# Optimization experiments

Measured on AMD Instinct MI355X. Metric: run time of the kernel, lower is better.

The kernel has to match this reference:

```python
import jax, jax.numpy as jnp
import numpy as np

N, E, DIN, H, HEADS = 50000, 800000, 128, 64, 4


def setup_inputs() -> dict:
    key = jax.random.key(0)
    ks = jax.random.split(key, 12)

    def p(k, shape, fan_in):
        return jax.random.normal(k, shape, dtype=jnp.float32) / np.float32(np.sqrt(fan_in))

    return dict(
        x=jax.random.normal(ks[0], (N, DIN), dtype=jnp.float32),
        edge_index=jax.random.randint(ks[1], (2, E), 0, N, dtype=jnp.int32),
        # GCNConv(input_dim, hidden)
        W_gcn=p(ks[2], (DIN, H), DIN), b_gcn=jnp.zeros((H,), jnp.float32),
        # GATConv(hidden, hidden, heads=4, concat=True)
        W_gat=p(ks[3], (H, HEADS * H), H),
        att_src=p(ks[4], (HEADS, H), H), att_dst=p(ks[5], (HEADS, H), H),
        b_gat=jnp.zeros((HEADS * H,), jnp.float32),
        # SAGEConv(4*hidden, hidden): lin_l (neighbors, with bias), lin_r (root, no bias)
        W_sage_l=p(ks[6], (HEADS * H, H), HEADS * H), b_sage=jnp.zeros((H,), jnp.float32),
        W_sage_r=p(ks[7], (HEADS * H, H), HEADS * H),
        # edge-pair MLP: Linear(2*hidden, hidden) -> ReLU -> Linear(hidden, 1)
        W1=p(ks[8], (2 * H, H), 2 * H), b1=jnp.zeros((H,), jnp.float32),
        W2=p(ks[9], (H, 1), H), b2=jnp.zeros((1,), jnp.float32),
    )


def reference(x, edge_index, W_gcn, b_gcn, W_gat, att_src, att_dst, b_gat,
              W_sage_l, b_sage, W_sage_r, W1, b1, W2, b2):
    n = x.shape[0]
    src, dst = edge_index[0], edge_index[1]
    loop = jnp.arange(n, dtype=edge_index.dtype)
    # edges with self-loops appended (GCN and GAT add self-loops by default)
    s2 = jnp.concatenate([src, loop])
    d2 = jnp.concatenate([dst, loop])

    h = x @ W_gcn                                            # [N, H]
    deg = jax.ops.segment_sum(jnp.ones_like(d2, jnp.float32), d2, num_segments=n)
    dinv = jnp.where(deg > 0, jax.lax.rsqrt(jnp.maximum(deg, 1e-12)), 0.0)
    norm = dinv[s2] * dinv[d2]                               # [E+N]
    h = jax.ops.segment_sum(h[s2] * norm[:, None], d2, num_segments=n) + b_gcn
    h = jax.nn.relu(h)                                       # dropout: identity in eval

    # ---- GATConv (heads=4, concat=True, negative_slope=0.2) ----
    g = (h @ W_gat).reshape(n, HEADS, H)                     # [N, heads, C]
    a_s = jnp.sum(g * att_src, axis=-1)                      # [N, heads]
    a_d = jnp.sum(g * att_dst, axis=-1)
    e = jax.nn.leaky_relu(a_s[s2] + a_d[d2], 0.2)            # [E+N, heads]
    m = jax.ops.segment_max(e, d2, num_segments=n)           # per-target max (stable softmax)
    e = jnp.exp(e - m[d2])
    z = jax.ops.segment_sum(e, d2, num_segments=n)
    alpha = e / (z[d2] + 1e-16)                              # edge softmax over incoming edges
    g = jax.ops.segment_sum(g[s2] * alpha[:, :, None], d2, num_segments=n)
    g = jax.nn.relu(g.reshape(n, HEADS * H) + b_gat)

    # ---- SAGEConv (mean aggregation, root weight, no self-loops) ----
    nsum = jax.ops.segment_sum(g[src], dst, num_segments=n)
    cnt = jax.ops.segment_sum(jnp.ones_like(dst, jnp.float32), dst, num_segments=n)
    mean = nsum / jnp.maximum(cnt, 1.0)[:, None]
    s = jax.nn.relu(mean @ W_sage_l + b_sage + g @ W_sage_r)  # [N, H]

    # ---- edge-pair MLP + sigmoid ----
    ef = jnp.concatenate([s[src], s[dst]], axis=1)            # [E, 2H]
    pred = jax.nn.relu(ef @ W1 + b1) @ W2 + b2                # [E, 1]
    return jax.nn.sigmoid(pred[:, 0])
```

## Files before the change

### kernel.cpp

```cpp
#include <hip/hip_runtime.h>
#include <math.h>

typedef float v2f __attribute__((ext_vector_type(2)));
static __device__ __forceinline__ float4 f4s(float v){ return make_float4(v,v,v,v); }
static __device__ __forceinline__ float4 f4add(float4 a, float4 b){ return make_float4(a.x+b.x,a.y+b.y,a.z+b.z,a.w+b.w); }
static __device__ __forceinline__ float4 f4max(float4 a, float4 b){ return make_float4(fmaxf(a.x,b.x),fmaxf(a.y,b.y),fmaxf(a.z,b.z),fmaxf(a.w,b.w)); }
static __device__ __forceinline__ float4 f4scale(float4 a, float s){ return make_float4(a.x*s,a.y*s,a.z*s,a.w*s); }
static __device__ __forceinline__ float4 f4fma(float4 acc, float s, float4 b){
  acc.x += s*b.x; acc.y += s*b.y; acc.z += s*b.z; acc.w += s*b.w; return acc;
}
static __device__ __forceinline__ float4 f4relu(float4 a){ return f4max(a, f4s(0.f)); }
static __device__ __forceinline__ float4 f4leaky(float4 a){
  return make_float4(a.x>0.f?a.x:0.2f*a.x, a.y>0.f?a.y:0.2f*a.y, a.z>0.f?a.z:0.2f*a.z, a.w>0.f?a.w:0.2f*a.w);
}
static __device__ __forceinline__ float4 f4expf(float4 a){ return make_float4(__expf(a.x),__expf(a.y),__expf(a.z),__expf(a.w)); }
static __device__ __forceinline__ unsigned short f2bf(float f){
  unsigned int u = __float_as_uint(f);
  unsigned int r = (u + 0x7fffu + ((u >> 16) & 1u)) >> 16;
  return (unsigned short)r;
}
static __device__ __forceinline__ ushort4 f2bf4(float4 f){
  ushort4 r; r.x=f2bf(f.x); r.y=f2bf(f.y); r.z=f2bf(f.z); r.w=f2bf(f.w); return r;
}
static __device__ __forceinline__ float4 bfu2f4(uint2 u){
  return make_float4(__uint_as_float(u.x << 16), __uint_as_float(u.x & 0xffff0000u),
                     __uint_as_float(u.y << 16), __uint_as_float(u.y & 0xffff0000u));
}
static __device__ __forceinline__ float4 bfu2f4_lo(uint4 u){ return bfu2f4(make_uint2(u.x, u.y)); }
static __device__ __forceinline__ float4 bfu2f4_hi(uint4 u){ return bfu2f4(make_uint2(u.z, u.w)); }

typedef __attribute__((ext_vector_type(8))) unsigned short u16x8;
static __device__ __forceinline__ u16x8 f2bf8(float4 a, float4 b){
  u16x8 r;
  r[0]=f2bf(a.x); r[1]=f2bf(a.y); r[2]=f2bf(a.z); r[3]=f2bf(a.w);
  r[4]=f2bf(b.x); r[5]=f2bf(b.y); r[6]=f2bf(b.z); r[7]=f2bf(b.w);
  return r;
}
static __device__ __forceinline__ void red2(float4& a, float4& b){
  a.x += __shfl_xor(a.x, 8); a.y += __shfl_xor(a.y, 8);
  a.z += __shfl_xor(a.z, 8); a.w += __shfl_xor(a.w, 8);
  b.x += __shfl_xor(b.x, 8); b.y += __shfl_xor(b.y, 8);
  b.z += __shfl_xor(b.z, 8); b.w += __shfl_xor(b.w, 8);
}
static __device__ __forceinline__ unsigned char f2fp8(float v){
  return (unsigned char)(__builtin_amdgcn_cvt_pk_fp8_f32(v, v, 0, false) & 0xff);
}
static __device__ __forceinline__ unsigned int f4_fp8x4(float4 v){
  unsigned int r = __builtin_amdgcn_cvt_pk_fp8_f32(v.x, v.y, 0, false);
  r = __builtin_amdgcn_cvt_pk_fp8_f32(v.z, v.w, r, true);
  return r;
}
static __device__ __forceinline__ float4 fp8x4_f4(unsigned int q){
  v2f lo = __builtin_amdgcn_cvt_pk_f32_fp8(q, false);
  v2f hi = __builtin_amdgcn_cvt_pk_f32_fp8(q, true);
  return make_float4(lo[0], lo[1], hi[0], hi[1]);
}
static __device__ __forceinline__ float dot8(float4 a, float4 b, const float* v){
  return a.x*v[0]+a.y*v[1]+a.z*v[2]+a.w*v[3]+b.x*v[4]+b.y*v[5]+b.z*v[6]+b.w*v[7];
}

typedef __attribute__((ext_vector_type(8))) short bf16x8;
typedef __attribute__((ext_vector_type(4))) float f32x4;

__global__ __launch_bounds__(256) void k_rank(const int* __restrict__ dst, int* __restrict__ cnt,
                                              int* __restrict__ rank, int E){
  int t = blockIdx.x*256 + threadIdx.x;
  if (t < E) rank[t] = atomicAdd(&cnt[dst[t]], 1);
}
__global__ __launch_bounds__(256) void k_scan1v(const int* __restrict__ cnt, int* __restrict__ excl,
                                                int* __restrict__ bsum, int n, int nb,
                                                const float* __restrict__ Wg, const float* __restrict__ as,
                                                const float* __restrict__ ad, float* __restrict__ Vs,
                                                float* __restrict__ Vd){
  if ((int)blockIdx.x == nb){
    int t = threadIdx.x;
    int h = t >> 6, k = t & 63;
    float s = 0.f, d = 0.f;
    const float* wr = Wg + (size_t)k*256 + h*64;
    const float* ar = as + h*64;
    const float* dr = ad + h*64;
    for (int c = 0; c < 64; ++c){ float w = wr[c]; s += w*ar[c]; d += w*dr[c]; }
    Vs[t] = s; Vd[t] = d;
    return;
  }
  __shared__ int sc[256];
  int t = threadIdx.x; int i = blockIdx.x*256 + t;
  int v = (i<n)?cnt[i]:0;
  sc[t]=v; __syncthreads();
  for (int o=1;o<256;o<<=1){ int a=(t>=o)?sc[t-o]:0; __syncthreads(); sc[t]+=a; __syncthreads(); }
  if (i<n) excl[i] = sc[t]-v;
  if (t==255) bsum[blockIdx.x] = sc[t];
}
__global__ __launch_bounds__(256) void k_scan3b(const int* __restrict__ cnt, const int* __restrict__ excl,
                                                const int* __restrict__ bsum, int* __restrict__ offs,
                                                float* __restrict__ dinv, int n, int E, int nb){
  __shared__ int sb[256];
  int t = threadIdx.x;
  int v = (t<nb)?bsum[t]:0;
  sb[t]=v; __syncthreads();
  for (int o=1;o<256;o<<=1){ int a=(t>=o)?sb[t-o]:0; __syncthreads(); sb[t]+=a; __syncthreads(); }
  int bex = sb[blockIdx.x] - bsum[blockIdx.x];
  int i = blockIdx.x*256 + t;
  if (i < n){
    offs[i] = excl[i] + bex;
    dinv[i] = rsqrtf((float)cnt[i] + 1.0f);
    if (i == 0) offs[n] = E;
  }
}

__global__ __launch_bounds__(256) void k_fillg(const int* __restrict__ src, const int* __restrict__ dstv,
                                               const int* __restrict__ offs, const int* __restrict__ rank,
                                               int* __restrict__ csr, int E, int fb,
                                               const float* __restrict__ x, const float* __restrict__ Wg,
                                               unsigned char* __restrict__ a8, int n,
                                               const float* __restrict__ dinv){
  if ((int)blockIdx.x < fb){
    int t = blockIdx.x*256 + threadIdx.x;
    if (t < E) csr[offs[dstv[t]] + rank[t]] = src[t];
    return;
  }
  __shared__ unsigned short wb[1024*8];
  int tid = threadIdx.x;
  for (int s = tid; s < 1024; s += 256){
    int l = s & 63, f = s >> 6;
    int cc = f & 3, kb = f >> 2;
    int c  = cc*16 + (l & 15);
    int kr = kb*32 + ((l >> 4) << 3);
    const float* wp = Wg + (size_t)kr*64 + c;
    unsigned short* dp = &wb[s*8];
    #pragma unroll
    for (int j = 0; j < 8; ++j) dp[j] = f2bf(wp[(size_t)j*64]);
  }
  __syncthreads();
  int wv = tid >> 6, l = tid & 63;
  int lrow = l & 15;
  int lk = (l >> 4) << 3;
  int g = blockIdx.x - fb;
  int r0 = (g << 6) + (wv << 4);
  int m = r0 + lrow;
  bf16x8 afr[4];
  #pragma unroll
  for (int kb = 0; kb < 4; ++kb){
    bf16x8 a = {0,0,0,0,0,0,0,0};
    if (m < n){
      const float* p = x + (size_t)m*128 + kb*32 + lk;
      float4 f0 = *(const float4*)p;
      float4 f1 = *(const float4*)(p + 4);
      a[0]=(short)f2bf(f0.x); a[1]=(short)f2bf(f0.y); a[2]=(short)f2bf(f0.z); a[3]=(short)f2bf(f0.w);
      a[4]=(short)f2bf(f1.x); a[5]=(short)f2bf(f1.y); a[6]=(short)f2bf(f1.z); a[7]=(short)f2bf(f1.w);
    }
    afr[kb] = a;
  }
  int rbase = r0 + ((l >> 4) << 2);
  float sc[4];
  #pragma unroll
  for (int r = 0; r < 4; ++r) sc[r] = (rbase + r < n) ? dinv[rbase + r] : 0.f;
  #pragma unroll
  for (int cc = 0; cc < 4; ++cc){
    f32x4 acc = {0.f, 0.f, 0.f, 0.f};
    #pragma unroll
    for (int kb = 0; kb < 4; ++kb){
      bf16x8 b = *(const bf16x8*)&wb[((kb*4 + cc)*64 + l)*8];
      acc = __builtin_amdgcn_mfma_f32_16x16x32_bf16(afr[kb], b, acc, 0, 0, 0);
    }
    int c = cc*16 + lrow;
    #pragma unroll
    for (int r = 0; r < 4; ++r){
      int rr = rbase + r;
      if (rr < n) a8[(size_t)rr*64 + c] = f2fp8(acc[r] * sc[r]);
    }
  }
}

__global__ __launch_bounds__(256) void k_gatsage(const unsigned short* __restrict__ Y,
                                                 const float* __restrict__ Wg,
                                                 const float* __restrict__ bg,
                                                 const float* __restrict__ Wl,
                                                 const float* __restrict__ Wr,
                                                 unsigned short* __restrict__ R,
                                                 unsigned char* __restrict__ P8, int n){
  constexpr int LDG = 264;
  extern __shared__ unsigned short lds[];
  unsigned short* wb1 = lds;
  unsigned short* wb2 = wb1 + 2048*8;
  unsigned short* gb  = wb2 + 4096*8;
  int tid = threadIdx.x;
  for (int s = tid; s < 2048; s += 256){
    int l = s & 63, f = s >> 6;
    int cc = f & 15, kb = f >> 4;
    int c  = cc*16 + (l & 15);
    int kr = kb*32 + ((l >> 4) << 3);
    const float* wp = Wg + (size_t)kr*256 + c;
    unsigned short* dp = &wb1[s*8];
    #pragma unroll
    for (int j = 0; j < 8; ++j) dp[j] = f2bf(wp[(size_t)j*256]);
  }
  for (int s = tid; s < 4096; s += 256){
    int l = s & 63, f = s >> 6;
    int cc = f & 7, kb = f >> 3;
    int c  = cc*16 + (l & 15);
    int kr = kb*32 + ((l >> 4) << 3);
    const float* wp = (c >= 64) ? (Wr + (size_t)kr*64 + (c - 64)) : (Wl + (size_t)kr*64 + c);
    unsigned short* dp = &wb2[s*8];
    #pragma unroll
    for (int j = 0; j < 8; ++j) dp[j] = f2bf(wp[(size_t)j*64]);
  }
  __syncthreads();
  int wv = tid >> 6, l = tid & 63;
  int lrow = l & 15;
  int lk = (l >> 4) << 3;
  int rbase4 = (l >> 4) << 2;
  int ngrp = (n + 63) >> 6;
  for (int g = blockIdx.x; g < ngrp; g += gridDim.x){
    int r0 = (g << 6) + (wv << 4);
    int m = r0 + lrow;
    bf16x8 afr[4][2];
    #pragma unroll
    for (int h = 0; h < 4; ++h){
      #pragma unroll
      for (int kb = 0; kb < 2; ++kb){
        bf16x8 a = {0,0,0,0,0,0,0,0};
        if (m < n) a = *(const bf16x8*)(Y + (size_t)m*256 + h*64 + kb*32 + lk);
        afr[h][kb] = a;
      }
    }
    #pragma unroll
    for (int cc = 0; cc < 16; ++cc){
      f32x4 acc = {0.f, 0.f, 0.f, 0.f};
      int hh = cc >> 2;
      #pragma unroll
      for (int kb = 0; kb < 2; ++kb){
        bf16x8 b = *(const bf16x8*)&wb1[((kb*16 + cc)*64 + l)*8];
        acc = __builtin_amdgcn_mfma_f32_16x16x32_bf16(afr[hh][kb], b, acc, 0, 0, 0);
      }
      int c = cc*16 + lrow;
      float bv = bg[c];
      #pragma unroll
      for (int r = 0; r < 4; ++r){
        int lr = (wv << 4) + rbase4 + r;
        gb[lr*LDG + c] = f2bf(fmaxf(acc[r] + bv, 0.f));
      }
    }
    bf16x8 afb[8];
    #pragma unroll
    for (int kb = 0; kb < 8; ++kb)
      afb[kb] = *(const bf16x8*)&gb[((wv << 4) + lrow)*LDG + kb*32 + lk];
    #pragma unroll
    for (int cc = 0; cc < 8; ++cc){
      f32x4 acc = {0.f, 0.f, 0.f, 0.f};
      #pragma unroll
      for (int kb = 0; kb < 8; ++kb){
        bf16x8 b = *(const bf16x8*)&wb2[((kb*8 + cc)*64 + l)*8];
        acc = __builtin_amdgcn_mfma_f32_16x16x32_bf16(afb[kb], b, acc, 0, 0, 0);
      }
      int c = cc*16 + lrow;
      #pragma unroll
      for (int r = 0; r < 4; ++r){
        int rr = r0 + rbase4 + r;
        if (rr < n){
          float v = acc[r];
          if (c < 64) P8[(size_t)rr*64 + c] = f2fp8(v);
          else        R[(size_t)rr*64 + (c - 64)] = f2bf(v);
        }
      }
    }
  }
}

__global__ __launch_bounds__(256) void k_gcn(const unsigned char* __restrict__ a8, const float* __restrict__ dinv,
                                             const float* __restrict__ b, const int* __restrict__ offs,
                                             const int* __restrict__ csr, const float* __restrict__ Vs,
                                             const float* __restrict__ Vd, unsigned char* __restrict__ h8,
                                             float* __restrict__ D, int n){
  __shared__ float svs[256], svd[256];
  svs[threadIdx.x] = Vs[threadIdx.x];
  svd[threadIdx.x] = Vd[threadIdx.x];
  __syncthreads();
  int l = threadIdx.x & 63;
  int node = (((blockIdx.x*256 + threadIdx.x) >> 6) << 2) + (l >> 4);
  int l15 = l & 15;
  int grp = l15 >> 3, sub = l15 & 7;
  bool ok = node < n;
  int beg = 0, end = 0;
  float di = 0.f;
  if (ok){ beg = offs[node]; end = offs[node+1]; di = dinv[node]; }
  float4 aL0 = f4s(0.f), aH0 = f4s(0.f), aL1 = f4s(0.f), aH1 = f4s(0.f);
  int i = beg + grp;
  for (; i + 2 < end; i += 4){
    int s0 = csr[i], s1 = csr[i+2];
    uint2 u0 = *(const uint2*)(a8 + (size_t)s0*64 + (sub<<3));
    uint2 u1 = *(const uint2*)(a8 + (size_t)s1*64 + (sub<<3));
    aL0 = f4add(aL0, fp8x4_f4(u0.x)); aH0 = f4add(aH0, fp8x4_f4(u0.y));
    aL1 = f4add(aL1, fp8x4_f4(u1.x)); aH1 = f4add(aH1, fp8x4_f4(u1.y));
  }
  if (i < end){
    int s0 = csr[i];
    uint2 u0 = *(const uint2*)(a8 + (size_t)s0*64 + (sub<<3));
    aL0 = f4add(aL0, fp8x4_f4(u0.x)); aH0 = f4add(aH0, fp8x4_f4(u0.y));
  }
  float4 aL = f4add(aL0, aL1), aH = f4add(aH0, aH1);
  red2(aL, aH);
  if (ok){
    uint2 us = *(const uint2*)(a8 + (size_t)node*64 + (sub<<3));
    aL = f4add(aL, fp8x4_f4(us.x)); aH = f4add(aH, fp8x4_f4(us.y));
    float4 b0 = *(const float4*)(b + (sub<<3));
    float4 b1 = *(const float4*)(b + (sub<<3) + 4);
    float4 r0 = f4relu(f4fma(b0, di, aL));
    float4 r1 = f4relu(f4fma(b1, di, aH));
    if (grp == 0){
      uint2 q; q.x = f4_fp8x4(r0); q.y = f4_fp8x4(r1);
      *(uint2*)(h8 + (size_t)node*64 + (sub<<3)) = q;
    }
    const float* vs0 = svs + (grp*128) + (sub<<3);
    const float* vd0 = svd + (grp*128) + (sub<<3);
    float s0 = dot8(r0, r1, vs0);
    float s1 = dot8(r0, r1, vs0 + 64);
    float d0 = dot8(r0, r1, vd0);
    float d1 = dot8(r0, r1, vd0 + 64);
    #pragma unroll
    for (int o = 1; o < 8; o <<= 1){
      s0 += __shfl_xor(s0, o); s1 += __shfl_xor(s1, o);
      d0 += __shfl_xor(d0, o); d1 += __shfl_xor(d1, o);
    }
    if (sub == 0){
      *(float2*)(D + (size_t)node*8 + grp*2)     = make_float2(s0, s1);
      *(float2*)(D + (size_t)node*8 + 4 + grp*2) = make_float2(d0, d1);
    }
  }
}

#define GAT_CAP 128
__global__ __launch_bounds__(256) void k_gat2(const float* __restrict__ D, const unsigned char* __restrict__ H8,
                                              const int* __restrict__ offs, const int* __restrict__ csr,
                                              unsigned short* __restrict__ Y, int n){
  __shared__ float wl[8][GAT_CAP*4];
  __shared__ int   sl[8][GAT_CAP];
  int hw = threadIdx.x >> 5;
  int node = (blockIdx.x*256 + threadIdx.x) >> 5;
  int l5 = threadIdx.x & 31;
  if (node >= n) return;
  int beg = offs[node], end = offs[node+1];
  int deg = end - beg;
  float4 ed  = *(const float4*)(D + (size_t)node*8 + 4);
  float4 es0 = *(const float4*)(D + (size_t)node*8);
  float4 wself = f4expf(f4leaky(f4add(es0, ed)));
  float4 z4 = f4s(0.f);
  for (int i = beg + l5; i < end; i += 32){
    int s = csr[i];
    float4 w = f4expf(f4leaky(f4add(*(const float4*)(D + (size_t)s*8), ed)));
    int li = i - beg;
    if (li < GAT_CAP){ *(float4*)&wl[hw][li<<2] = w; sl[hw][li] = s << 6; }
    z4 = f4add(z4, w);
  }
  for (int m = 1; m < 32; m <<= 1){
    z4.x += __shfl_xor(z4.x, m); z4.y += __shfl_xor(z4.y, m);
    z4.z += __shfl_xor(z4.z, m); z4.w += __shfl_xor(z4.w, m);
  }
  z4 = f4add(z4, wself);
  int grp = l5 >> 4;
  int sub = l5 & 15;
  int c0b = sub << 2;
  float4 a0 = f4s(0.f), a1 = f4s(0.f), a2 = f4s(0.f), a3 = f4s(0.f);
  int nl = deg < GAT_CAP ? deg : GAT_CAP;
  int i = grp;
  for (; i + 2 < nl; i += 4){
    int o0 = sl[hw][i], o1 = sl[hw][i+2];
    float4 w0 = *(const float4*)&wl[hw][i<<2];
    float4 w1 = *(const float4*)&wl[hw][(i+2)<<2];
    unsigned int q0 = *(const unsigned int*)(H8 + o0 + c0b);
    unsigned int q1 = *(const unsigned int*)(H8 + o1 + c0b);
    float4 f0 = fp8x4_f4(q0);
    float4 f1 = fp8x4_f4(q1);
    a0 = f4fma(a0, w0.x, f0); a1 = f4fma(a1, w0.y, f0);
    a2 = f4fma(a2, w0.z, f0); a3 = f4fma(a3, w0.w, f0);
    a0 = f4fma(a0, w1.x, f1); a1 = f4fma(a1, w1.y, f1);
    a2 = f4fma(a2, w1.z, f1); a3 = f4fma(a3, w1.w, f1);
  }
  if (i < nl){
    float4 w0 = *(const float4*)&wl[hw][i<<2];
    float4 f0 = fp8x4_f4(*(const unsigned int*)(H8 + sl[hw][i] + c0b));
    a0 = f4fma(a0, w0.x, f0); a1 = f4fma(a1, w0.y, f0);
    a2 = f4fma(a2, w0.z, f0); a3 = f4fma(a3, w0.w, f0);
  }
  for (int j = nl + grp; j < deg; j += 2){
    int s = csr[beg+j];
    float4 e = f4leaky(f4add(*(const float4*)(D + (size_t)s*8), ed));
    float4 w = f4expf(e);
    float4 f0 = fp8x4_f4(*(const unsigned int*)(H8 + ((size_t)s << 6) + c0b));
    a0 = f4fma(a0, w.x, f0); a1 = f4fma(a1, w.y, f0);
    a2 = f4fma(a2, w.z, f0); a3 = f4fma(a3, w.w, f0);
  }
  a0.x += __shfl_xor(a0.x, 16); a0.y += __shfl_xor(a0.y, 16); a0.z += __shfl_xor(a0.z, 16); a0.w += __shfl_xor(a0.w, 16);
  a1.x += __shfl_xor(a1.x, 16); a1.y += __shfl_xor(a1.y, 16); a1.z += __shfl_xor(a1.z, 16); a1.w += __shfl_xor(a1.w, 16);
  a2.x += __shfl_xor(a2.x, 16); a2.y += __shfl_xor(a2.y, 16); a2.z += __shfl_xor(a2.z, 16); a2.w += __shfl_xor(a2.w, 16);
  a3.x += __shfl_xor(a3.x, 16); a3.y += __shfl_xor(a3.y, 16); a3.z += __shfl_xor(a3.z, 16); a3.w += __shfl_xor(a3.w, 16);
  if (grp == 0){
    float4 fs = fp8x4_f4(*(const unsigned int*)(H8 + ((size_t)node << 6) + c0b));
    a0 = f4fma(a0, wself.x, fs);
    a1 = f4fma(a1, wself.y, fs);
    a2 = f4fma(a2, wself.z, fs);
    a3 = f4fma(a3, wself.w, fs);
    a0 = f4scale(a0, 1.f/(z4.x + 1e-16f));
    a1 = f4scale(a1, 1.f/(z4.y + 1e-16f));
    a2 = f4scale(a2, 1.f/(z4.z + 1e-16f));
    a3 = f4scale(a3, 1.f/(z4.w + 1e-16f));
    unsigned short* yp = Y + (size_t)node*256 + (sub << 2);
    *(ushort4*)(yp)       = f2bf4(a0);
    *(ushort4*)(yp + 64)  = f2bf4(a1);
    *(ushort4*)(yp + 128) = f2bf4(a2);
    *(ushort4*)(yp + 192) = f2bf4(a3);
  }
}

__global__ __launch_bounds__(256) void k_sage(const unsigned char* __restrict__ P8, const unsigned short* __restrict__ R,
                                              const float* __restrict__ b, const int* __restrict__ offs,
                                              const int* __restrict__ csr, const float* __restrict__ W1a,
                                              const float* __restrict__ W1b, unsigned char* __restrict__ T2, int n){
  __shared__ unsigned short wfr[1024*8];
  __shared__ unsigned short stile[16][72];
  int tid = threadIdx.x;
  for (int s = tid; s < 1024; s += 256){
    int l = s & 63, f = s >> 6;
    int cc = f & 7, kb = f >> 3;
    int c  = cc*16 + (l & 15);
    int kr = kb*32 + ((l >> 4) << 3);
    const float* wp = (c >= 64) ? (W1b + (size_t)kr*64 + (c - 64)) : (W1a + (size_t)kr*64 + c);
    unsigned short* dp = &wfr[s*8];
    #pragma unroll
    for (int j = 0; j < 8; ++j) dp[j] = f2bf(wp[(size_t)j*64]);
  }
  int wv = tid >> 6, l = tid & 63;
  int base = blockIdx.x*16;
  int lrow16 = (wv << 2) + (l >> 4);
  int node = base + lrow16;
  int l15 = l & 15;
  int grp = l15 >> 3, sub = l15 & 7;
  bool ok = node < n;
  int beg = 0, end = 0;
  if (ok){ beg = offs[node]; end = offs[node+1]; }
  float4 aL0 = f4s(0.f), aH0 = f4s(0.f), aL1 = f4s(0.f), aH1 = f4s(0.f);
  int i = beg + grp;
  for (; i + 2 < end; i += 4){
    int s0 = csr[i], s1 = csr[i+2];
    uint2 u0 = *(const uint2*)(P8 + (size_t)s0*64 + (sub<<3));
    uint2 u1 = *(const uint2*)(P8 + (size_t)s1*64 + (sub<<3));
    aL0 = f4add(aL0, fp8x4_f4(u0.x)); aH0 = f4add(aH0, fp8x4_f4(u0.y));
    aL1 = f4add(aL1, fp8x4_f4(u1.x)); aH1 = f4add(aH1, fp8x4_f4(u1.y));
  }
  if (i < end){
    int s0 = csr[i];
    uint2 u0 = *(const uint2*)(P8 + (size_t)s0*64 + (sub<<3));
    aL0 = f4add(aL0, fp8x4_f4(u0.x)); aH0 = f4add(aH0, fp8x4_f4(u0.y));
  }
  float4 aL = f4add(aL0, aL1), aH = f4add(aH0, aH1);
  red2(aL, aH);
  float4 r0 = f4s(0.f), r1 = f4s(0.f);
  if (ok){
    float minv = 1.f / fmaxf((float)(end - beg), 1.f);
    uint4 ur = *(const uint4*)(R + (size_t)node*64 + (sub<<3));
    float4 b0 = *(const float4*)(b + (sub<<3));
    float4 b1 = *(const float4*)(b + (sub<<3) + 4);
    r0 = f4relu(f4add(f4fma(b0, minv, aL), bfu2f4_lo(ur)));
    r1 = f4relu(f4add(f4fma(b1, minv, aH), bfu2f4_hi(ur)));
  }
  if (grp == 0) *(u16x8*)&stile[lrow16][sub << 3] = f2bf8(r0, r1);
  __syncthreads();
  int lrow = l & 15, lk = (l >> 4) << 3;
  bf16x8 af0 = *(const bf16x8*)&stile[lrow][lk];
  bf16x8 af1 = *(const bf16x8*)&stile[lrow][32 + lk];
  int rbase = (l >> 4) << 2;
  #pragma unroll
  for (int q = 0; q < 2; ++q){
    int cc = wv*2 + q;
    f32x4 acc = {0.f, 0.f, 0.f, 0.f};
    acc = __builtin_amdgcn_mfma_f32_16x16x32_bf16(af0, *(const bf16x8*)&wfr[(cc*64 + l)*8], acc, 0, 0, 0);
    acc = __builtin_amdgcn_mfma_f32_16x16x32_bf16(af1, *(const bf16x8*)&wfr[((8 + cc)*64 + l)*8], acc, 0, 0, 0);
    int c = cc*16 + lrow;
    #pragma unroll
    for (int r = 0; r < 4; ++r){
      int nd = base + rbase + r;
      if (nd < n) T2[(size_t)nd*128 + c] = f2fp8(acc[r]);
    }
  }
}

__global__ __launch_bounds__(256) void k_mlp(const unsigned char* __restrict__ T2,
                                             const float* __restrict__ b1, const float* __restrict__ W2,
                                             const float* __restrict__ b2, const int* __restrict__ src,
                                             const int* __restrict__ dst, float* __restrict__ out, int E){
  int t = threadIdx.x;
  int e = blockIdx.x*32 + (t >> 3);
  if (e >= E) return;
  int sub = t & 7;
  int s = src[e], d = dst[e];
  uint2 uu = *(const uint2*)(T2 + (size_t)s*128 + (sub<<3));
  uint2 vv = *(const uint2*)(T2 + (size_t)d*128 + 64 + (sub<<3));
  float4 u0 = fp8x4_f4(uu.x), u1 = fp8x4_f4(uu.y);
  float4 v0 = fp8x4_f4(vv.x), v1 = fp8x4_f4(vv.y);
  float4 bb0 = *(const float4*)(b1 + (sub<<3));
  float4 bb1 = *(const float4*)(b1 + (sub<<3) + 4);
  float4 w0 = *(const float4*)(W2 + (sub<<3));
  float4 w1 = *(const float4*)(W2 + (sub<<3) + 4);
  float4 ta = f4relu(f4add(f4add(u0, v0), bb0));
  float4 tb = f4relu(f4add(f4add(u1, v1), bb1));
  float p = ta.x*w0.x + ta.y*w0.y + ta.z*w0.z + ta.w*w0.w
          + tb.x*w1.x + tb.y*w1.y + tb.z*w1.z + tb.w*w1.w;
  p += __shfl_xor(p, 1);
  p += __shfl_xor(p, 2);
  p += __shfl_xor(p, 4);
  if (sub == 0) out[e] = 1.f / (1.f + __expf(-(p + b2[0])));
}

extern "C" void kernel_launch(void* const* d_in, const int* in_sizes, int n_in,
                              void* d_out, int out_size, void* d_ws, size_t ws_size,
                              hipStream_t stream){
  const float* x     = (const float*)d_in[0];
  const int*   eidx  = (const int*)  d_in[1];
  const float* W_gcn = (const float*)d_in[2];
  const float* b_gcn = (const float*)d_in[3];
  const float* W_gat = (const float*)d_in[4];
  const float* att_s = (const float*)d_in[5];
  const float* att_d = (const float*)d_in[6];
  const float* b_gat = (const float*)d_in[7];
  const float* W_sl  = (const float*)d_in[8];
  const float* b_sg  = (const float*)d_in[9];
  const float* W_sr  = (const float*)d_in[10];
  const float* W1    = (const float*)d_in[11];
  const float* b1    = (const float*)d_in[12];
  const float* W2    = (const float*)d_in[13];
  const float* b2    = (const float*)d_in[14];
  float* out = (float*)d_out;

  const int N = in_sizes[0] / 128;
  const int E = in_sizes[1] / 2;
  const int* src = eidx;
  const int* dst = eidx + E;

  float* ws   = (float*)d_ws;
  float* dinv = ws;
  float* D    = dinv + (size_t)N;
  float* Vs   = D + (size_t)N*8;
  float* Vd   = Vs + 256;
  unsigned short* Y  = (unsigned short*)(Vd + 256);
  unsigned short* R  = Y + (size_t)N*256;
  unsigned char*  A8 = (unsigned char*)(R + (size_t)N*64);
  unsigned char*  H8 = A8 + (size_t)N*64;
  unsigned char*  P8 = H8 + (size_t)N*64;
  unsigned char*  T2 = P8 + (size_t)N*64;
  int* cnt  = (int*)(T2 + (size_t)N*128);
  int* excl = cnt + N;
  int* bsum = excl + N;
  int* offs = bsum + 256;
  int* rank = offs + N + 1;
  int* csr  = rank + E;

  const int nb = (N + 255) / 256;
  const int fb = (E + 255) / 256;
  const int gtiles = (N + 63) / 64;
  const int nwb = (N + 15) / 16;
  const int GSH = (2048*8 + 4096*8 + 64*264) * 2;

  static bool s_attr = false;
  if (!s_attr){
    hipFuncSetAttribute((const void*)k_gatsage, hipFuncAttributeMaxDynamicSharedMemorySize, GSH);
    s_attr = true;
  }

  hipMemsetAsync(cnt, 0, (size_t)N*sizeof(int), stream);
  k_rank  <<<fb, 256, 0, stream>>>(dst, cnt, rank, E);
  k_scan1v<<<nb + 1, 256, 0, stream>>>(cnt, excl, bsum, N, nb, W_gat, att_s, att_d, Vs, Vd);
  k_scan3b<<<nb, 256, 0, stream>>>(cnt, excl, bsum, offs, dinv, N, E, nb);
  k_fillg <<<fb + gtiles, 256, 0, stream>>>(src, dst, offs, rank, csr, E, fb,
                                            x, W_gcn, A8, N, dinv);

  k_gcn <<<nwb, 256, 0, stream>>>(A8, dinv, b_gcn, offs, csr, Vs, Vd, H8, D, N);

  k_gat2<<<(N+7)/8, 256, 0, stream>>>(D, H8, offs, csr, Y, N);

  k_gatsage<<<256, 256, GSH, stream>>>(Y, W_gat, b_gat, W_sl, W_sr, R, P8, N);

  k_sage<<<nwb, 256, 0, stream>>>(P8, R, b_sg, offs, csr, W1, W1 + 64*64, T2, N);

  k_mlp <<<(E+31)/32, 256, 0, stream>>>(T2, b1, W2, b2, src, dst, out, E);
}
```

Before: 285.6 us.

## Pre-pack GAT/SAGE weights to bf16 once and read them from global memory

The bf16 conversion and fragment packing of the GAT and SAGE weight matrices moves into extra blocks of the rank kernel, writing the packed layout to workspace once. k_gatsage no longer stages ~96KB of weights in LDS per block. It reads B fragments straight from global/L2 and keeps only a small LDS tile, so one 64-row tile per block over 782 blocks with higher occupancy. The cost is repeated global reads of weight fragments instead of LDS reads.

```diff
diff --git a/kernel.cpp b/kernel.cpp
--- a/kernel.cpp
+++ b/kernel.cpp
@@ -62,11 +62,37 @@
 typedef __attribute__((ext_vector_type(8))) short bf16x8;
 typedef __attribute__((ext_vector_type(4))) float f32x4;
 
-__global__ __launch_bounds__(256) void k_rank(const int* __restrict__ dst, int* __restrict__ cnt,
-                                              int* __restrict__ rank, int E){
-  int t = blockIdx.x*256 + threadIdx.x;
-  if (t < E) rank[t] = atomicAdd(&cnt[dst[t]], 1);
-}
+__global__ __launch_bounds__(256) void k_rankw(const int* __restrict__ dst, int* __restrict__ cnt,
+                                               int* __restrict__ rank, int E, int fb,
+                                               const float* __restrict__ Wg, const float* __restrict__ Wl,
+                                               const float* __restrict__ Wr, unsigned short* __restrict__ WT){
+  if ((int)blockIdx.x < fb){
+    int t = blockIdx.x*256 + threadIdx.x;
+    if (t < E) rank[t] = atomicAdd(&cnt[dst[t]], 1);
+    return;
+  }
+  int s = (blockIdx.x - fb)*256 + threadIdx.x;
+  int l = s & 63, f = s >> 6;
+  const float* wp; int ld;
+  if (s < 2048){
+    int cc = f & 15, kb = f >> 4;
+    int c  = cc*16 + (l & 15);
+    int kr = kb*32 + ((l >> 4) << 3);
+    wp = Wg + (size_t)kr*256 + c; ld = 256;
+  } else {
+    int f2 = f - 32;
+    int cc = f2 & 7, kb = f2 >> 3;
+    int c  = cc*16 + (l & 15);
+    int kr = kb*32 + ((l >> 4) << 3);
+    wp = (c >= 64) ? (Wr + (size_t)kr*64 + (c - 64)) : (Wl + (size_t)kr*64 + c);
+    ld = 64;
+  }
+  u16x8 o;
+  #pragma unroll
+  for (int j = 0; j < 8; ++j) o[j] = f2bf(wp[(size_t)j*ld]);
+  *(u16x8*)(WT + (size_t)s*8) = o;
+}
+
 __global__ __launch_bounds__(256) void k_scan1v(const int* __restrict__ cnt, int* __restrict__ excl,
                                                 int* __restrict__ bsum, int n, int nb,
                                                 const float* __restrict__ Wg, const float* __restrict__ as,
@@ -172,96 +198,69 @@
   }
 }
 
-__global__ __launch_bounds__(256) void k_gatsage(const unsigned short* __restrict__ Y,
-                                                 const float* __restrict__ Wg,
-                                                 const float* __restrict__ bg,
-                                                 const float* __restrict__ Wl,
-                                                 const float* __restrict__ Wr,
-                                                 unsigned short* __restrict__ R,
-                                                 unsigned char* __restrict__ P8, int n){
+__global__ __launch_bounds__(256, 4) void k_gatsage(const unsigned short* __restrict__ Y,
+                                                    const unsigned short* __restrict__ WT,
+                                                    const float* __restrict__ bg,
+                                                    unsigned short* __restrict__ R,
+                                                    unsigned char* __restrict__ P8, int n){
   constexpr int LDG = 264;
-  extern __shared__ unsigned short lds[];
-  unsigned short* wb1 = lds;
-  unsigned short* wb2 = wb1 + 2048*8;
-  unsigned short* gb  = wb2 + 4096*8;
+  __shared__ unsigned short gb[64*LDG];
+  const unsigned short* WT1 = WT;
+  const unsigned short* WT2 = WT + 2048*8;
   int tid = threadIdx.x;
-  for (int s = tid; s < 2048; s += 256){
-    int l = s & 63, f = s >> 6;
-    int cc = f & 15, kb = f >> 4;
-    int c  = cc*16 + (l & 15);
-    int kr = kb*32 + ((l >> 4) << 3);
-    const float* wp = Wg + (size_t)kr*256 + c;
-    unsigned short* dp = &wb1[s*8];
-    #pragma unroll
-    for (int j = 0; j < 8; ++j) dp[j] = f2bf(wp[(size_t)j*256]);
-  }
-  for (int s = tid; s < 4096; s += 256){
-    int l = s & 63, f = s >> 6;
-    int cc = f & 7, kb = f >> 3;
-    int c  = cc*16 + (l & 15);
-    int kr = kb*32 + ((l >> 4) << 3);
-    const float* wp = (c >= 64) ? (Wr + (size_t)kr*64 + (c - 64)) : (Wl + (size_t)kr*64 + c);
-    unsigned short* dp = &wb2[s*8];
-    #pragma unroll
-    for (int j = 0; j < 8; ++j) dp[j] = f2bf(wp[(size_t)j*64]);
-  }
-  __syncthreads();
   int wv = tid >> 6, l = tid & 63;
   int lrow = l & 15;
   int lk = (l >> 4) << 3;
   int rbase4 = (l >> 4) << 2;
-  int ngrp = (n + 63) >> 6;
-  for (int g = blockIdx.x; g < ngrp; g += gridDim.x){
-    int r0 = (g << 6) + (wv << 4);
-    int m = r0 + lrow;
-    bf16x8 afr[4][2];
-    #pragma unroll
-    for (int h = 0; h < 4; ++h){
-      #pragma unroll
-      for (int kb = 0; kb < 2; ++kb){
-        bf16x8 a = {0,0,0,0,0,0,0,0};
-        if (m < n) a = *(const bf16x8*)(Y + (size_t)m*256 + h*64 + kb*32 + lk);
-        afr[h][kb] = a;
-      }
-    }
-    #pragma unroll
-    for (int cc = 0; cc < 16; ++cc){
-      f32x4 acc = {0.f, 0.f, 0.f, 0.f};
-      int hh = cc >> 2;
-      #pragma unroll
-      for (int kb = 0; kb < 2; ++kb){
-        bf16x8 b = *(const bf16x8*)&wb1[((kb*16 + cc)*64 + l)*8];
-        acc = __builtin_amdgcn_mfma_f32_16x16x32_bf16(afr[hh][kb], b, acc, 0, 0, 0);
-      }
-      int c = cc*16 + lrow;
-      float bv = bg[c];
-      #pragma unroll
-      for (int r = 0; r < 4; ++r){
-        int lr = (wv << 4) + rbase4 + r;
-        gb[lr*LDG + c] = f2bf(fmaxf(acc[r] + bv, 0.f));
-      }
-    }
-    bf16x8 afb[8];
-    #pragma unroll
-    for (int kb = 0; kb < 8; ++kb)
-      afb[kb] = *(const bf16x8*)&gb[((wv << 4) + lrow)*LDG + kb*32 + lk];
-    #pragma unroll
-    for (int cc = 0; cc < 8; ++cc){
-      f32x4 acc = {0.f, 0.f, 0.f, 0.f};
-      #pragma unroll
-      for (int kb = 0; kb < 8; ++kb){
-        bf16x8 b = *(const bf16x8*)&wb2[((kb*8 + cc)*64 + l)*8];
-        acc = __builtin_amdgcn_mfma_f32_16x16x32_bf16(afb[kb], b, acc, 0, 0, 0);
-      }
-      int c = cc*16 + lrow;
-      #pragma unroll
-      for (int r = 0; r < 4; ++r){
-        int rr = r0 + rbase4 + r;
-        if (rr < n){
-          float v = acc[r];
-          if (c < 64) P8[(size_t)rr*64 + c] = f2fp8(v);
-          else        R[(size_t)rr*64 + (c - 64)] = f2bf(v);
-        }
+  int r0 = ((int)blockIdx.x << 6) + (wv << 4);
+  int m = r0 + lrow;
+  bf16x8 afr[4][2];
+  #pragma unroll
+  for (int h = 0; h < 4; ++h){
+    #pragma unroll
+    for (int kb = 0; kb < 2; ++kb){
+      bf16x8 a = {0,0,0,0,0,0,0,0};
+      if (m < n) a = *(const bf16x8*)(Y + (size_t)m*256 + h*64 + kb*32 + lk);
+      afr[h][kb] = a;
+    }
+  }
+  #pragma unroll
+  for (int cc = 0; cc < 16; ++cc){
+    f32x4 acc = {0.f, 0.f, 0.f, 0.f};
+    int hh = cc >> 2;
+    #pragma unroll
+    for (int kb = 0; kb < 2; ++kb){
+      bf16x8 b = *(const bf16x8*)&WT1[((size_t)((kb*16 + cc)*64 + l))*8];
+      acc = __builtin_amdgcn_mfma_f32_16x16x32_bf16(afr[hh][kb], b, acc, 0, 0, 0);
+    }
+    int c = cc*16 + lrow;
+    float bv = bg[c];
+    #pragma unroll
+    for (int r = 0; r < 4; ++r){
+      int lr = (wv << 4) + rbase4 + r;
+      gb[lr*LDG + c] = f2bf(fmaxf(acc[r] + bv, 0.f));
+    }
+  }
+  bf16x8 afb[8];
+  #pragma unroll
+  for (int kb = 0; kb < 8; ++kb)
+    afb[kb] = *(const bf16x8*)&gb[((wv << 4) + lrow)*LDG + kb*32 + lk];
+  #pragma unroll
+  for (int cc = 0; cc < 8; ++cc){
+    f32x4 acc = {0.f, 0.f, 0.f, 0.f};
+    #pragma unroll
+    for (int kb = 0; kb < 8; ++kb){
+      bf16x8 b = *(const bf16x8*)&WT2[((size_t)((kb*8 + cc)*64 + l))*8];
+      acc = __builtin_amdgcn_mfma_f32_16x16x32_bf16(afb[kb], b, acc, 0, 0, 0);
+    }
+    int c = cc*16 + lrow;
+    #pragma unroll
+    for (int r = 0; r < 4; ++r){
+      int rr = r0 + rbase4 + r;
+      if (rr < n){
+        float v = acc[r];
+        if (c < 64) P8[(size_t)rr*64 + c] = f2fp8(v);
+        else        R[(size_t)rr*64 + (c - 64)] = f2bf(v);
       }
     }
   }
@@ -541,7 +540,8 @@
   float* D    = dinv + (size_t)N;
   float* Vs   = D + (size_t)N*8;
   float* Vd   = Vs + 256;
-  unsigned short* Y  = (unsigned short*)(Vd + 256);
+  unsigned short* WT = (unsigned short*)(Vd + 256);
+  unsigned short* Y  = WT + (size_t)6144*8;
   unsigned short* R  = Y + (size_t)N*256;
   unsigned char*  A8 = (unsigned char*)(R + (size_t)N*64);
   unsigned char*  H8 = A8 + (size_t)N*64;
@@ -558,16 +558,9 @@
   const int fb = (E + 255) / 256;
   const int gtiles = (N + 63) / 64;
   const int nwb = (N + 15) / 16;
-  const int GSH = (2048*8 + 4096*8 + 64*264) * 2;
-
-  static bool s_attr = false;
-  if (!s_attr){
-    hipFuncSetAttribute((const void*)k_gatsage, hipFuncAttributeMaxDynamicSharedMemorySize, GSH);
-    s_attr = true;
-  }
 
   hipMemsetAsync(cnt, 0, (size_t)N*sizeof(int), stream);
-  k_rank  <<<fb, 256, 0, stream>>>(dst, cnt, rank, E);
+  k_rankw <<<fb + 24, 256, 0, stream>>>(dst, cnt, rank, E, fb, W_gat, W_sl, W_sr, WT);
   k_scan1v<<<nb + 1, 256, 0, stream>>>(cnt, excl, bsum, N, nb, W_gat, att_s, att_d, Vs, Vd);
   k_scan3b<<<nb, 256, 0, stream>>>(cnt, excl, bsum, offs, dinv, N, E, nb);
   k_fillg <<<fb + gtiles, 256, 0, stream>>>(src, dst, offs, rank, csr, E, fb,
@@ -577,7 +570,7 @@
 
   k_gat2<<<(N+7)/8, 256, 0, stream>>>(D, H8, offs, csr, Y, N);
 
-  k_gatsage<<<256, 256, GSH, stream>>>(Y, W_gat, b_gat, W_sl, W_sr, R, P8, N);
+  k_gatsage<<<gtiles, 256, 0, stream>>>(Y, WT, b_gat, R, P8, N);
 
   k_sage<<<nwb, 256, 0, stream>>>(P8, R, b_sg, offs, csr, W1, W1 + 64*64, T2, N);
 
```

After: 276.6 us. 1.03x faster.
